# Performance work log

Measured on AMD Instinct MI355X. Metric: run time of the kernel, lower is better.

The kernel has to match this reference:

```python
import jax, jax.numpy as jnp
import numpy as np
import math

_INV_SQRT2 = 1.0 / math.sqrt(2.0)
B, N, D, H = 4, 8192, 1024, 16
DH = D // H  # 64
GH = 4 * DH  # 256


def setup_inputs() -> dict:
    key = jax.random.key(0)
    ks = jax.random.split(key, 8)
    std = 0.02
    return {
        "x": jax.random.normal(ks[0], (B, N, D), jnp.float32),
        "w_q": jax.random.normal(ks[1], (D, D), jnp.float32) * std,
        "w_v": jax.random.normal(ks[2], (D, D), jnp.float32) * std,
        "w_o": jax.random.normal(ks[3], (D, D), jnp.float32) * std,
        "ln_g": jnp.ones((DH,), jnp.float32),
        "ln_b": jnp.zeros((DH,), jnp.float32),
        "gate_w1": jax.random.normal(ks[4], (DH, GH), jnp.float32) * std,
        "gate_w2": jax.random.normal(ks[5], (GH, 2 * N), jnp.float32) * std,
        "wrm_w1": jax.random.normal(ks[6], (DH, GH), jnp.float32) * std,
        "wrm_w2": jax.random.normal(ks[7], (GH, N), jnp.float32) * std,
    }


def reference(x, w_q, w_v, w_o, ln_g, ln_b, gate_w1, gate_w2, wrm_w1, wrm_w2):
    b, n, d = x.shape
    h, dh = H, DH
    # projections -> (b, h, n, dh)
    q = (x @ w_q).reshape(b, n, h, dh).transpose(0, 2, 1, 3)
    v = (x @ w_v).reshape(b, n, h, dh).transpose(0, 2, 1, 3)
    # per-head summary query + LayerNorm (biased variance, eps=1e-5)
    bar_q = q.mean(axis=2)  # (b, h, dh)
    mu = bar_q.mean(axis=-1, keepdims=True)
    var = ((bar_q - mu) ** 2).mean(axis=-1, keepdims=True)
    bar_q = (bar_q - mu) / jnp.sqrt(var + 1e-5) * ln_g + ln_b
    # complex spectral gate: (b, h, 2n) -> real || imag
    g_raw = jax.nn.gelu(bar_q @ gate_w1, approximate=False) @ gate_w2
    g = g_raw[..., :n] + 1j * g_raw[..., n:]  # (b, h, n) complex
    # FFT -> gate -> IFFT along sequence axis
    v_hat = jnp.fft.fft(v, axis=2) * g[..., None]
    v_tilde = jnp.fft.ifft(v_hat, axis=2).real.astype(x.dtype)
    # Haar wavelet refinement
    even, odd = v_tilde[..., 0::2, :], v_tilde[..., 1::2, :]
    w_hat = jnp.concatenate([(even + odd) * _INV_SQRT2,
                             (even - odd) * _INV_SQRT2], axis=-2)
    s = (jax.nn.gelu(bar_q @ wrm_w1, approximate=False) @ wrm_w2)[..., None]
    w_hat = w_hat * s
    half = n // 2
    low, high = w_hat[..., :half, :], w_hat[..., half:, :]
    ev = (low + high) * _INV_SQRT2
    od = (low - high) * _INV_SQRT2
    v_ref = jnp.stack([ev, od], axis=-2).reshape(b, h, n, dh)  # interleave even/odd
    v_tilde = v_tilde + v_ref
    y = v_tilde.transpose(0, 2, 1, 3).reshape(b, n, d)
    return y @ w_o
```

## Files before the change

### kernel.cpp

```cpp
#include <hip/hip_runtime.h>
#include <hip/hip_bf16.h>
#include <math.h>

#define PB 4
#define PN 8192
#define PD 1024
#define PH 16
#define PDH 64
#define PGH 256

typedef __bf16 bf16x8 __attribute__((ext_vector_type(8)));
typedef __bf16 bf16x2 __attribute__((ext_vector_type(2)));
typedef float f32x4 __attribute__((ext_vector_type(4)));
typedef unsigned int u32;
typedef unsigned short u16;

typedef __attribute__((address_space(3))) void lds_void_t;
typedef const __attribute__((address_space(1))) void gbl_void_t;
#define ASYNC_COPY16(gp, lp) \
    __builtin_amdgcn_global_load_lds((gbl_void_t*)(gp), (lds_void_t*)(lp), 16, 0, 0)

__device__ inline float gelu_exact(float x) {
    return 0.5f * x * (1.0f + erff(x * 0.70710678118654752440f));
}

__device__ inline float2 f2(float x, float y) { return make_float2(x, y); }
__device__ inline float2 cadd(float2 a, float2 b) { return f2(a.x + b.x, a.y + b.y); }
__device__ inline float2 csub(float2 a, float2 b) { return f2(a.x - b.x, a.y - b.y); }
__device__ inline float2 cmul(float2 a, float2 b) {
    return f2(a.x * b.x - a.y * b.y, a.x * b.y + a.y * b.x);
}

#define PHYS(i) ((i) ^ (((i) >> 4) & 15))

__device__ inline u32 packbf(float a, float b) {
    __bf16 ba = (__bf16)a, bb = (__bf16)b;
    return (u32)(*(u16*)&ba) | ((u32)(*(u16*)&bb) << 16);
}

__global__ void convert_reduce(const float* __restrict__ x, __bf16* __restrict__ xb,
                               float* __restrict__ xsum) {
    int b = blockIdx.z;
    int d = blockIdx.y * 256 + threadIdx.x;
    int n0 = blockIdx.x * 256;
    const float* p = x + ((size_t)b * PN + n0) * PD + d;
    __bf16* q = xb + ((size_t)b * PN + n0) * PD + d;
    float s = 0.0f;
    #pragma unroll 4
    for (int i = 0; i < 256; i++) {
        float v = p[(size_t)i * PD];
        s += v;
        q[(size_t)i * PD] = (__bf16)v;
    }
    atomicAdd(&xsum[b * PD + d], s);
}

__global__ void transpose_w(const float* __restrict__ wv, const float* __restrict__ wo,
                            __bf16* __restrict__ wvt, __bf16* __restrict__ wot) {
    __shared__ float t[64][65];
    const float* src = blockIdx.z ? wo : wv;
    __bf16* dst = blockIdx.z ? wot : wvt;
    int r0 = blockIdx.y * 64, c0 = blockIdx.x * 64;
    int lr = threadIdx.x >> 6, lc = threadIdx.x & 63;
    #pragma unroll
    for (int i = 0; i < 16; i++)
        t[lr + 4 * i][lc] = src[(size_t)(r0 + lr + 4 * i) * PD + c0 + lc];
    __syncthreads();
    #pragma unroll
    for (int i = 0; i < 16; i++)
        dst[(size_t)(c0 + lr + 4 * i) * PD + r0 + lc] = (__bf16)t[lc][lr + 4 * i];
}

__global__ void barq_ln(const float* __restrict__ xsum, const float* __restrict__ w_q,
                        const float* __restrict__ ln_g, const float* __restrict__ ln_b,
                        float* __restrict__ bar_ln) {
    int b = blockIdx.y;
    int lane = threadIdx.x & 63;
    int w = threadIdx.x >> 6;
    int c = blockIdx.x * 64 + lane;
    const float* xs = xsum + b * PD + w * 256;
    const float* wq = w_q + (size_t)(w * 256) * PD + c;
    float acc = 0.0f;
    for (int k = 0; k < 256; k++) acc += xs[k] * wq[(size_t)k * PD];
    __shared__ float part[4][64];
    part[w][lane] = acc;
    __syncthreads();
    if (w == 0) {
        float bar = (part[0][lane] + part[1][lane] + part[2][lane] + part[3][lane])
                    * (1.0f / (float)PN);
        float mu = bar;
        for (int o = 32; o > 0; o >>= 1) mu += __shfl_xor(mu, o, 64);
        mu *= (1.0f / 64.0f);
        float d0 = bar - mu;
        float vv = d0 * d0;
        for (int o = 32; o > 0; o >>= 1) vv += __shfl_xor(vv, o, 64);
        vv *= (1.0f / 64.0f);
        bar_ln[b * PD + c] = d0 * rsqrtf(vv + 1e-5f) * ln_g[lane] + ln_b[lane];
    }
}

__global__ void small1(const float* __restrict__ bar_ln, const float* __restrict__ gw1,
                       const float* __restrict__ ww1, float* __restrict__ tg,
                       float* __restrict__ tw) {
    int bh = blockIdx.x;
    int j = threadIdx.x;
    __shared__ float bl[PDH];
    if (j < PDH) bl[j] = bar_ln[bh * PDH + j];
    __syncthreads();
    float a1 = 0.0f, a2 = 0.0f;
    for (int k = 0; k < PDH; k++) {
        float bv = bl[k];
        a1 += bv * gw1[k * PGH + j];
        a2 += bv * ww1[k * PGH + j];
    }
    tg[bh * PGH + j] = gelu_exact(a1);
    tw[bh * PGH + j] = gelu_exact(a2);
}

__global__ void small2(const float* __restrict__ tg, const float* __restrict__ tw,
                       const float* __restrict__ gw2, const float* __restrict__ ww2,
                       float* __restrict__ g_raw, float* __restrict__ s_full) {
    int chunk = blockIdx.x;
    int bh0 = blockIdx.y * 8;
    bool isg = chunk < 64;
    const float* t = isg ? tg : tw;
    const float* w2 = isg ? gw2 : ww2;
    int stride = isg ? (2 * PN) : PN;
    int col = (isg ? chunk : chunk - 64) * 256 + threadIdx.x;
    __shared__ float tl[8][PGH];
    #pragma unroll
    for (int i = 0; i < 8; i++) tl[i][threadIdx.x] = t[(bh0 + i) * PGH + threadIdx.x];
    __syncthreads();
    float acc[8] = {0, 0, 0, 0, 0, 0, 0, 0};
    for (int k = 0; k < PGH; k++) {
        float w = w2[(size_t)k * stride + col];
        #pragma unroll
        for (int i = 0; i < 8; i++) acc[i] += tl[i][k] * w;
    }
    #pragma unroll
    for (int i = 0; i < 8; i++) {
        if (isg) g_raw[(size_t)(bh0 + i) * (2 * PN) + col] = acc[i];
        else     s_full[(size_t)(bh0 + i) * PN + col] = acc[i];
    }
}

__device__ inline void xcd_swizzle(int& tileM, int& tileN) {
    int lin = blockIdx.x + (blockIdx.y << 3);
    int xcd = lin & 7;
    int idx = lin >> 3;
    int yy = (xcd << 5) + (idx >> 3);
    int xx = idx & 7;
    tileM = yy << 7;
    tileN = xx << 7;
}

__global__ __launch_bounds__(256) void gemm_pair(const __bf16* __restrict__ A,
                                                 const __bf16* __restrict__ Bt,
                                                 u32* __restrict__ vt) {
    constexpr int K = PD, LDK = 32;
    __shared__ __attribute__((aligned(16))) __bf16 As[128 * LDK];
    __shared__ __attribute__((aligned(16))) __bf16 Bs[128 * LDK];
    const int tid = threadIdx.x;
    const int lane = tid & 63;
    const int wave = tid >> 6;
    const int wm = (wave >> 1) << 6;
    const int wn = (wave & 1) << 6;
    int tileM, tileN;
    xcd_swizzle(tileM, tileN);
    const int r = tid >> 2;
    const int cg = tid & 3;
    const int mrow = lane & 15;
    const int k0 = (lane >> 4) << 3;

    f32x4 acc[4][4] = {};
    const __bf16* Aptr = A + (size_t)(tileM + r) * K + cg * 8;
    const __bf16* Bptr = Bt + (size_t)(tileN + r) * K + cg * 8;

    for (int kt = 0; kt < K; kt += 32) {
        __syncthreads();
        ASYNC_COPY16(Aptr + kt,                  As + tid * 8);
        ASYNC_COPY16(Aptr + (size_t)64 * K + kt, As + 64 * LDK + tid * 8);
        ASYNC_COPY16(Bptr + kt,                  Bs + tid * 8);
        ASYNC_COPY16(Bptr + (size_t)64 * K + kt, Bs + 64 * LDK + tid * 8);
        __syncthreads();
        bf16x8 af[4], bfr[4];
        #pragma unroll
        for (int i = 0; i < 4; i++) af[i]  = *(const bf16x8*)&As[(wm + i * 16 + mrow) * LDK + k0];
        #pragma unroll
        for (int j = 0; j < 4; j++) bfr[j] = *(const bf16x8*)&Bs[(wn + j * 16 + mrow) * LDK + k0];
        #pragma unroll
        for (int i = 0; i < 4; i++)
            #pragma unroll
            for (int j = 0; j < 4; j++)
                acc[i][j] = __builtin_amdgcn_mfma_f32_16x16x32_bf16(af[i], bfr[j], acc[i][j], 0, 0, 0);
    }

    const int rq = (lane >> 4) << 2;
    const bool evl = (lane & 1) == 0;
    #pragma unroll
    for (int i = 0; i < 4; i++) {
        int grow = tileM + wm + i * 16 + rq;
        int b = grow >> 13;
        int nb = grow & 8191;
        #pragma unroll
        for (int j = 0; j < 4; j++) {
            u32 w[4];
            #pragma unroll
            for (int rr = 0; rr < 4; rr++) {
                float a = acc[i][j][rr];
                float o = __shfl_xor(a, 1, 64);
                w[rr] = packbf(a, o);
            }
            if (evl) {
                int col = tileN + wn + j * 16 + mrow;
                size_t idx = ((size_t)b * 512 + (col >> 1)) * PN + nb;
                *(uint4*)(vt + idx) = make_uint4(w[0], w[1], w[2], w[3]);
            }
        }
    }
}

__global__ __launch_bounds__(256) void gemm_ta(const u32* __restrict__ yt,
                                               const __bf16* __restrict__ Bt,
                                               float* __restrict__ Cf) {
    constexpr int K = PD, Nc = PD, LDKA = 40, LDKB = 32;
    __shared__ __attribute__((aligned(16))) __bf16 As[128 * LDKA];
    __shared__ __attribute__((aligned(16))) __bf16 Bs[128 * LDKB];
    u32* As32 = (u32*)As;
    const int tid = threadIdx.x;
    const int lane = tid & 63;
    const int wave = tid >> 6;
    const int wm = (wave >> 1) << 6;
    const int wn = (wave & 1) << 6;
    int tileM, tileN;
    xcd_swizzle(tileM, tileN);
    const int r = tid >> 2;
    const int cg = tid & 3;
    const int mrow = lane & 15;
    const int k0 = (lane >> 4) << 3;
    const int prow = tid & 7;
    const int seg = tid >> 3;

    const int b = tileM >> 13;
    const int n0 = tileM & 8191;
    const u32* abase = yt + ((size_t)b * 512 + prow) * PN + n0 + seg * 4;
    const __bf16* Bptr = Bt + (size_t)(tileN + r) * K + cg * 8;

    f32x4 acc[4][4] = {};
    uint4 pa0 = *(const uint4*)(abase);
    uint4 pa1 = *(const uint4*)(abase + (size_t)8 * PN);

    for (int kt = 0; kt < K; kt += 32) {
        __syncthreads();
        {
            int m0 = seg * 4;
            As32[(m0 + 0) * 20 + prow] = pa0.x;
            As32[(m0 + 1) * 20 + prow] = pa0.y;
            As32[(m0 + 2) * 20 + prow] = pa0.z;
            As32[(m0 + 3) * 20 + prow] = pa0.w;
            As32[(m0 + 0) * 20 + prow + 8] = pa1.x;
            As32[(m0 + 1) * 20 + prow + 8] = pa1.y;
            As32[(m0 + 2) * 20 + prow + 8] = pa1.z;
            As32[(m0 + 3) * 20 + prow + 8] = pa1.w;
        }
        ASYNC_COPY16(Bptr + kt,                  Bs + tid * 8);
        ASYNC_COPY16(Bptr + (size_t)64 * K + kt, Bs + 64 * LDKB + tid * 8);
        if (kt + 32 < K) {
            const u32* nxt = abase + (size_t)((kt >> 1) + 16) * PN;
            pa0 = *(const uint4*)(nxt);
            pa1 = *(const uint4*)(nxt + (size_t)8 * PN);
        }
        __syncthreads();
        bf16x8 af[4], bfr[4];
        #pragma unroll
        for (int i = 0; i < 4; i++) af[i]  = *(const bf16x8*)&As[(wm + i * 16 + mrow) * LDKA + k0];
        #pragma unroll
        for (int j = 0; j < 4; j++) bfr[j] = *(const bf16x8*)&Bs[(wn + j * 16 + mrow) * LDKB + k0];
        #pragma unroll
        for (int i = 0; i < 4; i++)
            #pragma unroll
            for (int j = 0; j < 4; j++)
                acc[i][j] = __builtin_amdgcn_mfma_f32_16x16x32_bf16(af[i], bfr[j], acc[i][j], 0, 0, 0);
    }

    const int rq = (lane >> 4) << 2;
    #pragma unroll
    for (int i = 0; i < 4; i++) {
        #pragma unroll
        for (int rr = 0; rr < 4; rr++) {
            int row = tileM + wm + i * 16 + rq + rr;
            size_t base = (size_t)row * Nc + tileN + wn + mrow;
            #pragma unroll
            for (int j = 0; j < 4; j++) Cf[base + j * 16] = acc[i][j][rr];
        }
    }
}

__global__ __launch_bounds__(512) void fftconv(const u32* __restrict__ vt,
                                               const float* __restrict__ g_raw,
                                               const float* __restrict__ s_full,
                                               u32* __restrict__ yt) {
    __shared__ float2 Z[PN];
    const int tid = threadIdx.x;
    const int row = blockIdx.x;
    const int bh = row >> 5;
    const u32* vp = vt + (size_t)row * PN;

    #pragma unroll
    for (int it = 0; it < 2; it++) {
        int n0 = (tid + it * 512) * 8;
        uint4 u0 = *(const uint4*)(vp + n0);
        uint4 u1 = *(const uint4*)(vp + n0 + 4);
        u32 uu[8] = {u0.x, u0.y, u0.z, u0.w, u1.x, u1.y, u1.z, u1.w};
        #pragma unroll
        for (int m = 0; m < 8; m++) {
            bf16x2 p = *(bf16x2*)&uu[m];
            Z[PHYS(n0 + m)] = f2((float)p.x, (float)p.y);
        }
    }
    __syncthreads();

    #pragma unroll
    for (int si = 0; si < 6; si++) {
        const int s = 11 - 2 * si;
        const int h = 1 << s;
        const float ang = -6.283185307179586f / (float)(4 * h);
        float sn, cs;
        __sincosf(ang * (float)(tid & (h - 1)), &sn, &cs);
        float2 w2 = f2(cs, sn);
        #pragma unroll
        for (int it = 0; it < 4; it++) {
            int q = tid + it * 512;
            int i = ((q >> s) << (s + 2)) + (q & (h - 1));
            float2 w1 = cmul(w2, w2);
            float2 a = Z[PHYS(i)],         bb = Z[PHYS(i + h)];
            float2 c = Z[PHYS(i + 2 * h)], d  = Z[PHYS(i + 3 * h)];
            float2 A0 = cadd(a, c);
            float2 C0 = cmul(csub(a, c), w2);
            float2 B0 = cadd(bb, d);
            float2 t  = cmul(csub(bb, d), w2);
            float2 D0 = f2(t.y, -t.x);
            Z[PHYS(i)]         = cadd(A0, B0);
            Z[PHYS(i + h)]     = cmul(csub(A0, B0), w1);
            Z[PHYS(i + 2 * h)] = cadd(C0, D0);
            Z[PHYS(i + 3 * h)] = cmul(csub(C0, D0), w1);
            if (h == 2048) w2 = cmul(w2, f2(0.92387953251f, -0.38268343236f));
        }
        __syncthreads();
    }
    #pragma unroll
    for (int it = 0; it < 8; it++) {
        int i = 2 * (tid + it * 512);
        float2 u = Z[PHYS(i)], t = Z[PHYS(i + 1)];
        Z[PHYS(i)]     = cadd(u, t);
        Z[PHYS(i + 1)] = csub(u, t);
    }
    __syncthreads();

    const float* gr = g_raw + (size_t)bh * (2 * PN);
    const float* gi = gr + PN;
    for (int m = tid; m < PN / 2 + 1; m += 512) {
        int p  = (m < PN / 2) ? 2 * m : 1;
        int k  = __brev((unsigned)p) >> 19;
        int Nk = (PN - k) & (PN - 1);
        int qd = __brev((unsigned)Nk) >> 19;
        float2 Za = Z[PHYS(p)], Zb = Z[PHYS(qd)];
        float v1r = 0.5f * (Za.x + Zb.x), v1i = 0.5f * (Za.y - Zb.y);
        float v2r = 0.5f * (Za.y + Zb.y), v2i = 0.5f * (Zb.x - Za.x);
        float grk = gr[k],  gik = gi[k];
        float grn = gr[Nk], gin = gi[Nk];
        float y1r  = v1r * grk - v1i * gik, y1i  = v1r * gik + v1i * grk;
        float y2r  = v2r * grk - v2i * gik, y2i  = v2r * gik + v2i * grk;
        float y1nr = v1r * grn + v1i * gin, y1ni = v1r * gin - v1i * grn;
        float y2nr = v2r * grn + v2i * gin, y2ni = v2r * gin - v2i * grn;
        float ys1r = 0.5f * (y1r + y1nr), ys1i = 0.5f * (y1i - y1ni);
        float ys2r = 0.5f * (y2r + y2nr), ys2i = 0.5f * (y2i - y2ni);
        Z[PHYS(p)] = f2(ys1r - ys2i, ys1i + ys2r);
        if (qd != p) Z[PHYS(qd)] = f2(ys1r + ys2i, ys2r - ys1i);
    }
    __syncthreads();

    #pragma unroll
    for (int si = 0; si < 6; si++) {
        const int s = 2 * si;
        const int h = 1 << s;
        const float ang = 6.283185307179586f / (float)(4 * h);
        float sn, cs;
        __sincosf(ang * (float)(tid & (h - 1)), &sn, &cs);
        float2 w2a = f2(cs, sn);
        float2 w2b = (h == 1024) ? cmul(w2a, f2(0.70710678119f, 0.70710678119f)) : w2a;
        #pragma unroll
        for (int it = 0; it < 4; it++) {
            int q = tid + it * 512;
            int i = ((q >> s) << (s + 2)) + (q & (h - 1));
            float2 w2 = (it & 1) ? w2b : w2a;
            float2 w1 = cmul(w2, w2);
            float2 a = Z[PHYS(i)],         bb = Z[PHYS(i + h)];
            float2 c = Z[PHYS(i + 2 * h)], d  = Z[PHYS(i + 3 * h)];
            float2 tb = cmul(bb, w1);
            float2 p0 = cadd(a, tb), p1 = csub(a, tb);
            float2 td = cmul(d, w1);
            float2 q0 = cadd(c, td), q1 = csub(c, td);
            float2 wq0 = cmul(q0, w2);
            float2 e   = cmul(q1, w2);
            float2 ei  = f2(-e.y, e.x);
            Z[PHYS(i)]         = cadd(p0, wq0);
            Z[PHYS(i + 2 * h)] = csub(p0, wq0);
            Z[PHYS(i + h)]     = cadd(p1, ei);
            Z[PHYS(i + 3 * h)] = csub(p1, ei);
        }
        __syncthreads();
    }
    {
        const float ang = 6.283185307179586f / (float)PN;
        float sn, cs;
        __sincosf(ang * (float)tid, &sn, &cs);
        float2 w = f2(cs, sn);
        #pragma unroll
        for (int it = 0; it < 8; it++) {
            int q = tid + it * 512;
            float2 u = Z[PHYS(q)];
            float2 t = cmul(Z[PHYS(q + PN / 2)], w);
            Z[PHYS(q)]          = cadd(u, t);
            Z[PHYS(q + PN / 2)] = csub(u, t);
            w = cmul(w, f2(0.92387953251f, 0.38268343236f));
        }
    }
    __syncthreads();

    const float* sp = s_full + (size_t)bh * PN;
    u32* yp = yt + (size_t)row * PN;
    const float inv = 1.0f / (float)PN;
    const float I2 = 0.70710678118654752440f;
    #pragma unroll
    for (int it = 0; it < 2; it++) {
        int nb = tid + it * 512;
        int n0 = nb * 8;
        int np0 = nb * 4;
        u32 ou[8];
        #pragma unroll
        for (int pp = 0; pp < 4; pp++) {
            float2 z0 = Z[PHYS(n0 + 2 * pp)];
            float2 z1 = Z[PHYS(n0 + 2 * pp + 1)];
            float s0  = sp[np0 + pp];
            float s1v = sp[np0 + pp + PN / 2];
            float ax = z0.x * inv, ay = z0.y * inv;
            float bx = z1.x * inv, by = z1.y * inv;
            float wlx = (ax + bx) * I2 * s0, whx = (ax - bx) * I2 * s1v;
            float evx = (wlx + whx) * I2,   odx = (wlx - whx) * I2;
            float wly = (ay + by) * I2 * s0, why = (ay - by) * I2 * s1v;
            float evy = (wly + why) * I2,   ody = (wly - why) * I2;
            ou[2 * pp]     = packbf(ax + evx, ay + evy);
            ou[2 * pp + 1] = packbf(bx + odx, by + ody);
        }
        *(uint4*)(yp + n0)     = make_uint4(ou[0], ou[1], ou[2], ou[3]);
        *(uint4*)(yp + n0 + 4) = make_uint4(ou[4], ou[5], ou[6], ou[7]);
    }
}

extern "C" void kernel_launch(void* const* d_in, const int* in_sizes, int n_in,
                              void* d_out, int out_size, void* d_ws, size_t ws_size,
                              hipStream_t stream) {
    const float* x    = (const float*)d_in[0];
    const float* w_q  = (const float*)d_in[1];
    const float* w_v  = (const float*)d_in[2];
    const float* w_o  = (const float*)d_in[3];
    const float* ln_g = (const float*)d_in[4];
    const float* ln_b = (const float*)d_in[5];
    const float* gw1  = (const float*)d_in[6];
    const float* gw2  = (const float*)d_in[7];
    const float* ww1  = (const float*)d_in[8];
    const float* ww2  = (const float*)d_in[9];
    float* out = (float*)d_out;

    const size_t XE = (size_t)PB * PN * PD;
    __bf16* xb   = (__bf16*)d_ws;
    __bf16* vb   = xb + XE;
    __bf16* wvt  = vb + XE;
    __bf16* wot  = wvt + (size_t)PD * PD;
    float*  xsum = (float*)(wot + (size_t)PD * PD);
    float*  bar  = xsum + PB * PD;
    float*  tg   = bar + PB * PD;
    float*  tw   = tg + 64 * PGH;
    float*  graw = tw + 64 * PGH;
    float*  sful = graw + (size_t)64 * 2 * PN;

    hipMemsetAsync(xsum, 0, PB * PD * sizeof(float), stream);

    convert_reduce<<<dim3(PN / 256, PD / 256, PB), 256, 0, stream>>>(x, xb, xsum);
    transpose_w<<<dim3(16, 16, 2), 256, 0, stream>>>(w_v, w_o, wvt, wot);
    barq_ln<<<dim3(PD / 64, PB), 256, 0, stream>>>(xsum, w_q, ln_g, ln_b, bar);
    small1<<<PB * PH, 256, 0, stream>>>(bar, gw1, ww1, tg, tw);
    small2<<<dim3(96, 8), 256, 0, stream>>>(tg, tw, gw2, ww2, graw, sful);
    gemm_pair<<<dim3(PD / 128, PB * PN / 128), 256, 0, stream>>>(xb, wvt, (u32*)vb);
    fftconv<<<PB * 512, 512, 0, stream>>>((const u32*)vb, graw, sful, (u32*)xb);
    gemm_ta<<<dim3(PD / 128, PB * PN / 128), 256, 0, stream>>>((const u32*)xb, wot, out);
}
```

Measured before the change: 679.9 us.

## Double-buffer LDS in both GEMMs and vectorize the convert-reduce kernel

Both bf16 MFMA GEMMs now use two LDS buffers. The next K-tile's async global-to-LDS copy is issued before the current tile's MFMAs, so only one barrier per iteration remains instead of two. Separately, the fp32-to-bf16 conversion kernel now reads 8 floats per thread with float4 loads and writes bf16x8 stores, reducing two rows per block through LDS before issuing fewer atomics. Risks are doubled LDS use per block, which may lower occupancy, and reliance on correct waits for the async copies before the barrier.

```diff
diff --git a/kernel.cpp b/kernel.cpp
--- a/kernel.cpp
+++ b/kernel.cpp
@@ -41,18 +41,34 @@
 __global__ void convert_reduce(const float* __restrict__ x, __bf16* __restrict__ xb,
                                float* __restrict__ xsum) {
     int b = blockIdx.z;
-    int d = blockIdx.y * 256 + threadIdx.x;
-    int n0 = blockIdx.x * 256;
-    const float* p = x + ((size_t)b * PN + n0) * PD + d;
-    __bf16* q = xb + ((size_t)b * PN + n0) * PD + d;
-    float s = 0.0f;
-    #pragma unroll 4
-    for (int i = 0; i < 256; i++) {
-        float v = p[(size_t)i * PD];
-        s += v;
-        q[(size_t)i * PD] = (__bf16)v;
-    }
-    atomicAdd(&xsum[b * PD + d], s);
+    int r = threadIdx.x >> 7;
+    int dt = threadIdx.x & 127;
+    int dq = dt * 8;
+    int nbase = blockIdx.x * 128;
+    float s[8] = {0, 0, 0, 0, 0, 0, 0, 0};
+    for (int i = 0; i < 64; i++) {
+        size_t row = (size_t)b * PN + nbase + i * 2 + r;
+        const float* p = x + row * PD + dq;
+        float4 f0 = *(const float4*)p;
+        float4 f1 = *(const float4*)(p + 4);
+        bf16x8 o;
+        o[0] = (__bf16)f0.x; o[1] = (__bf16)f0.y; o[2] = (__bf16)f0.z; o[3] = (__bf16)f0.w;
+        o[4] = (__bf16)f1.x; o[5] = (__bf16)f1.y; o[6] = (__bf16)f1.z; o[7] = (__bf16)f1.w;
+        s[0] += f0.x; s[1] += f0.y; s[2] += f0.z; s[3] += f0.w;
+        s[4] += f1.x; s[5] += f1.y; s[6] += f1.z; s[7] += f1.w;
+        *(bf16x8*)(xb + row * PD + dq) = o;
+    }
+    __shared__ float red[128][9];
+    if (r == 1) {
+        #pragma unroll
+        for (int j = 0; j < 8; j++) red[dt][j] = s[j];
+    }
+    __syncthreads();
+    if (r == 0) {
+        #pragma unroll
+        for (int j = 0; j < 8; j++)
+            atomicAdd(&xsum[b * PD + dq + j], s[j] + red[dt][j]);
+    }
 }
 
 __global__ void transpose_w(const float* __restrict__ wv, const float* __restrict__ wo,
@@ -158,8 +174,8 @@
                                                  const __bf16* __restrict__ Bt,
                                                  u32* __restrict__ vt) {
     constexpr int K = PD, LDK = 32;
-    __shared__ __attribute__((aligned(16))) __bf16 As[128 * LDK];
-    __shared__ __attribute__((aligned(16))) __bf16 Bs[128 * LDK];
+    __shared__ __attribute__((aligned(16))) __bf16 As[2][128 * LDK];
+    __shared__ __attribute__((aligned(16))) __bf16 Bs[2][128 * LDK];
     const int tid = threadIdx.x;
     const int lane = tid & 63;
     const int wave = tid >> 6;
@@ -176,23 +192,32 @@
     const __bf16* Aptr = A + (size_t)(tileM + r) * K + cg * 8;
     const __bf16* Bptr = Bt + (size_t)(tileN + r) * K + cg * 8;
 
+    ASYNC_COPY16(Aptr,                  &As[0][tid * 8]);
+    ASYNC_COPY16(Aptr + (size_t)64 * K, &As[0][64 * LDK + tid * 8]);
+    ASYNC_COPY16(Bptr,                  &Bs[0][tid * 8]);
+    ASYNC_COPY16(Bptr + (size_t)64 * K, &Bs[0][64 * LDK + tid * 8]);
+    __syncthreads();
+
+    int cur = 0;
     for (int kt = 0; kt < K; kt += 32) {
-        __syncthreads();
-        ASYNC_COPY16(Aptr + kt,                  As + tid * 8);
-        ASYNC_COPY16(Aptr + (size_t)64 * K + kt, As + 64 * LDK + tid * 8);
-        ASYNC_COPY16(Bptr + kt,                  Bs + tid * 8);
-        ASYNC_COPY16(Bptr + (size_t)64 * K + kt, Bs + 64 * LDK + tid * 8);
-        __syncthreads();
+        if (kt + 32 < K) {
+            ASYNC_COPY16(Aptr + kt + 32,                  &As[cur ^ 1][tid * 8]);
+            ASYNC_COPY16(Aptr + (size_t)64 * K + kt + 32, &As[cur ^ 1][64 * LDK + tid * 8]);
+            ASYNC_COPY16(Bptr + kt + 32,                  &Bs[cur ^ 1][tid * 8]);
+            ASYNC_COPY16(Bptr + (size_t)64 * K + kt + 32, &Bs[cur ^ 1][64 * LDK + tid * 8]);
+        }
         bf16x8 af[4], bfr[4];
         #pragma unroll
-        for (int i = 0; i < 4; i++) af[i]  = *(const bf16x8*)&As[(wm + i * 16 + mrow) * LDK + k0];
-        #pragma unroll
-        for (int j = 0; j < 4; j++) bfr[j] = *(const bf16x8*)&Bs[(wn + j * 16 + mrow) * LDK + k0];
+        for (int i = 0; i < 4; i++) af[i]  = *(const bf16x8*)&As[cur][(wm + i * 16 + mrow) * LDK + k0];
+        #pragma unroll
+        for (int j = 0; j < 4; j++) bfr[j] = *(const bf16x8*)&Bs[cur][(wn + j * 16 + mrow) * LDK + k0];
         #pragma unroll
         for (int i = 0; i < 4; i++)
             #pragma unroll
             for (int j = 0; j < 4; j++)
                 acc[i][j] = __builtin_amdgcn_mfma_f32_16x16x32_bf16(af[i], bfr[j], acc[i][j], 0, 0, 0);
+        __syncthreads();
+        cur ^= 1;
     }
 
     const int rq = (lane >> 4) << 2;
@@ -224,9 +249,8 @@
                                                const __bf16* __restrict__ Bt,
                                                float* __restrict__ Cf) {
     constexpr int K = PD, Nc = PD, LDKA = 40, LDKB = 32;
-    __shared__ __attribute__((aligned(16))) __bf16 As[128 * LDKA];
-    __shared__ __attribute__((aligned(16))) __bf16 Bs[128 * LDKB];
-    u32* As32 = (u32*)As;
+    __shared__ __attribute__((aligned(16))) __bf16 As[2][128 * LDKA];
+    __shared__ __attribute__((aligned(16))) __bf16 Bs[2][128 * LDKB];
     const int tid = threadIdx.x;
     const int lane = tid & 63;
     const int wave = tid >> 6;
@@ -240,6 +264,7 @@
     const int k0 = (lane >> 4) << 3;
     const int prow = tid & 7;
     const int seg = tid >> 3;
+    const int m0 = seg * 4;
 
     const int b = tileM >> 13;
     const int n0 = tileM & 8191;
@@ -247,40 +272,58 @@
     const __bf16* Bptr = Bt + (size_t)(tileN + r) * K + cg * 8;
 
     f32x4 acc[4][4] = {};
+
     uint4 pa0 = *(const uint4*)(abase);
     uint4 pa1 = *(const uint4*)(abase + (size_t)8 * PN);
-
+    {
+        u32* a32 = (u32*)&As[0][0];
+        a32[(m0 + 0) * 20 + prow] = pa0.x;
+        a32[(m0 + 1) * 20 + prow] = pa0.y;
+        a32[(m0 + 2) * 20 + prow] = pa0.z;
+        a32[(m0 + 3) * 20 + prow] = pa0.w;
+        a32[(m0 + 0) * 20 + prow + 8] = pa1.x;
+        a32[(m0 + 1) * 20 + prow + 8] = pa1.y;
+        a32[(m0 + 2) * 20 + prow + 8] = pa1.z;
+        a32[(m0 + 3) * 20 + prow + 8] = pa1.w;
+    }
+    ASYNC_COPY16(Bptr,                  &Bs[0][tid * 8]);
+    ASYNC_COPY16(Bptr + (size_t)64 * K, &Bs[0][64 * LDKB + tid * 8]);
+    pa0 = *(const uint4*)(abase + (size_t)16 * PN);
+    pa1 = *(const uint4*)(abase + (size_t)24 * PN);
+    __syncthreads();
+
+    int cur = 0;
     for (int kt = 0; kt < K; kt += 32) {
-        __syncthreads();
-        {
-            int m0 = seg * 4;
-            As32[(m0 + 0) * 20 + prow] = pa0.x;
-            As32[(m0 + 1) * 20 + prow] = pa0.y;
-            As32[(m0 + 2) * 20 + prow] = pa0.z;
-            As32[(m0 + 3) * 20 + prow] = pa0.w;
-            As32[(m0 + 0) * 20 + prow + 8] = pa1.x;
-            As32[(m0 + 1) * 20 + prow + 8] = pa1.y;
-            As32[(m0 + 2) * 20 + prow + 8] = pa1.z;
-            As32[(m0 + 3) * 20 + prow + 8] = pa1.w;
-        }
-        ASYNC_COPY16(Bptr + kt,                  Bs + tid * 8);
-        ASYNC_COPY16(Bptr + (size_t)64 * K + kt, Bs + 64 * LDKB + tid * 8);
         if (kt + 32 < K) {
-            const u32* nxt = abase + (size_t)((kt >> 1) + 16) * PN;
-            pa0 = *(const uint4*)(nxt);
-            pa1 = *(const uint4*)(nxt + (size_t)8 * PN);
-        }
-        __syncthreads();
+            u32* a32 = (u32*)&As[cur ^ 1][0];
+            a32[(m0 + 0) * 20 + prow] = pa0.x;
+            a32[(m0 + 1) * 20 + prow] = pa0.y;
+            a32[(m0 + 2) * 20 + prow] = pa0.z;
+            a32[(m0 + 3) * 20 + prow] = pa0.w;
+            a32[(m0 + 0) * 20 + prow + 8] = pa1.x;
+            a32[(m0 + 1) * 20 + prow + 8] = pa1.y;
+            a32[(m0 + 2) * 20 + prow + 8] = pa1.z;
+            a32[(m0 + 3) * 20 + prow + 8] = pa1.w;
+            ASYNC_COPY16(Bptr + kt + 32,                  &Bs[cur ^ 1][tid * 8]);
+            ASYNC_COPY16(Bptr + (size_t)64 * K + kt + 32, &Bs[cur ^ 1][64 * LDKB + tid * 8]);
+            if (kt + 64 < K) {
+                const u32* nxt = abase + (size_t)((kt >> 1) + 32) * PN;
+                pa0 = *(const uint4*)(nxt);
+                pa1 = *(const uint4*)(nxt + (size_t)8 * PN);
+            }
+        }
         bf16x8 af[4], bfr[4];
         #pragma unroll
-        for (int i = 0; i < 4; i++) af[i]  = *(const bf16x8*)&As[(wm + i * 16 + mrow) * LDKA + k0];
-        #pragma unroll
-        for (int j = 0; j < 4; j++) bfr[j] = *(const bf16x8*)&Bs[(wn + j * 16 + mrow) * LDKB + k0];
+        for (int i = 0; i < 4; i++) af[i]  = *(const bf16x8*)&As[cur][(wm + i * 16 + mrow) * LDKA + k0];
+        #pragma unroll
+        for (int j = 0; j < 4; j++) bfr[j] = *(const bf16x8*)&Bs[cur][(wn + j * 16 + mrow) * LDKB + k0];
         #pragma unroll
         for (int i = 0; i < 4; i++)
             #pragma unroll
             for (int j = 0; j < 4; j++)
                 acc[i][j] = __builtin_amdgcn_mfma_f32_16x16x32_bf16(af[i], bfr[j], acc[i][j], 0, 0, 0);
+        __syncthreads();
+        cur ^= 1;
     }
 
     const int rq = (lane >> 4) << 2;
@@ -487,7 +530,7 @@
 
     hipMemsetAsync(xsum, 0, PB * PD * sizeof(float), stream);
 
-    convert_reduce<<<dim3(PN / 256, PD / 256, PB), 256, 0, stream>>>(x, xb, xsum);
+    convert_reduce<<<dim3(PN / 128, 1, PB), 256, 0, stream>>>(x, xb, xsum);
     transpose_w<<<dim3(16, 16, 2), 256, 0, stream>>>(w_v, w_o, wvt, wot);
     barq_ln<<<dim3(PD / 64, PB), 256, 0, stream>>>(xsum, w_q, ln_g, ln_b, bar);
     small1<<<PB * PH, 256, 0, stream>>>(bar, gw1, ww1, tg, tw);
```

After: 664.8 us. 1.02x faster.
